# Kernel tuning notes

Measured on AMD Instinct MI355X. Metric: run time of the kernel, lower is better.

Reference implementation:

```python
import jax, jax.numpy as jnp
import numpy as np

D_MODEL = 1024
N_HEADS = 16
D_HEAD = D_MODEL // N_HEADS
D_FF = 4096
B, T = 2, 2048


def setup_inputs() -> dict:
    key = jax.random.key(0)
    ks = jax.random.split(key, 7)
    s = lambda fan_in: 1.0 / np.sqrt(fan_in)
    return {
        "x": jax.random.normal(ks[0], (B, T, D_MODEL), dtype=jnp.float32),
        "ln1_g": jnp.ones((D_MODEL,), jnp.float32),
        "ln1_b": jnp.zeros((D_MODEL,), jnp.float32),
        "w_qkv": jax.random.normal(ks[1], (D_MODEL, 3 * D_MODEL), jnp.float32) * s(D_MODEL),
        "w_proj": jax.random.normal(ks[2], (D_MODEL, D_MODEL), jnp.float32) * s(D_MODEL),
        "ln2_g": jnp.ones((D_MODEL,), jnp.float32),
        "ln2_b": jnp.zeros((D_MODEL,), jnp.float32),
        "w_fc1": jax.random.normal(ks[3], (D_MODEL, D_FF), jnp.float32) * s(D_MODEL),
        "w_fc2": jax.random.normal(ks[4], (D_FF, D_MODEL), jnp.float32) * s(D_FF),
    }


def _layernorm(x, g, b, eps=1e-5):
    mu = jnp.mean(x, axis=-1, keepdims=True)
    var = jnp.var(x, axis=-1, keepdims=True)
    return (x - mu) * jax.lax.rsqrt(var + eps) * g + b


def _attn(x, w_qkv, w_proj):
    Bx, Tx, d = x.shape
    qkv = x @ w_qkv  # [B,T,3d]
    q, k, v = jnp.split(qkv, 3, axis=-1)
    split = lambda t: t.reshape(Bx, Tx, N_HEADS, D_HEAD).transpose(0, 2, 1, 3)
    q, k, v = split(q), split(k), split(v)
    scores = jnp.einsum("bhqd,bhkd->bhqk", q, k) / np.sqrt(D_HEAD).astype(np.float32)
    mask = jnp.tril(jnp.ones((Tx, Tx), dtype=bool))
    scores = jnp.where(mask, scores, -jnp.inf)
    attn = jax.nn.softmax(scores, axis=-1)
    out = jnp.einsum("bhqk,bhkd->bhqd", attn, v)
    out = out.transpose(0, 2, 1, 3).reshape(Bx, Tx, d)
    return out @ w_proj


def reference(x, ln1_g, ln1_b, w_qkv, w_proj, ln2_g, ln2_b, w_fc1, w_fc2):
    x = x + _attn(_layernorm(x, ln1_g, ln1_b), w_qkv, w_proj)
    h = jax.nn.gelu(_layernorm(x, ln2_g, ln2_b) @ w_fc1, approximate=False)
    return x + h @ w_fc2
```

## Files before the change

### kernel.cpp

```cpp
#include <hip/hip_runtime.h>
#include <math.h>

using short8 = __attribute__((ext_vector_type(8))) short;
using f32x4  = __attribute__((ext_vector_type(4))) float;
typedef unsigned short ushort;

__device__ inline ushort f2bf(float f) {
    union { float f; unsigned int i; } v; v.f = f;
    unsigned int x = v.i;
    return (ushort)((x + 0x7FFFu + ((x >> 16) & 1u)) >> 16);
}
__device__ inline void st_out(float* p, float v) { *p = v; }
__device__ inline void st_out(ushort* p, float v) { *p = f2bf(v); }

__device__ inline void gl_lds16(const ushort* g, ushort* l) {
    __builtin_amdgcn_global_load_lds((const __attribute__((address_space(1))) unsigned int*)g,
                                     (__attribute__((address_space(3))) unsigned int*)l, 16, 0, 0);
}
#define MFMA __builtin_amdgcn_mfma_f32_16x16x32_bf16

__global__ __launch_bounds__(256) void ln_kernel(const float* __restrict__ x,
                                                 const float* __restrict__ g,
                                                 const float* __restrict__ b,
                                                 ushort* __restrict__ y) {
    int row = blockIdx.x;
    const float* xr = x + (size_t)row * 1024;
    int t = threadIdx.x;
    float v[4];
    float s = 0.f, s2 = 0.f;
#pragma unroll
    for (int i = 0; i < 4; i++) {
        v[i] = xr[t + i * 256];
        s += v[i]; s2 += v[i] * v[i];
    }
#pragma unroll
    for (int off = 1; off < 64; off <<= 1) {
        s += __shfl_xor(s, off); s2 += __shfl_xor(s2, off);
    }
    __shared__ float ps[8];
    int w = t >> 6;
    if ((t & 63) == 0) { ps[w] = s; ps[4 + w] = s2; }
    __syncthreads();
    s  = ps[0] + ps[1] + ps[2] + ps[3];
    s2 = ps[4] + ps[5] + ps[6] + ps[7];
    float mu   = s * (1.0f / 1024.0f);
    float var  = s2 * (1.0f / 1024.0f) - mu * mu;
    float rinv = rsqrtf(var + 1e-5f);
    ushort* yr = y + (size_t)row * 1024;
#pragma unroll
    for (int i = 0; i < 4; i++) {
        int c = t + i * 256;
        yr[c] = f2bf((v[i] - mu) * rinv * g[c] + b[c]);
    }
}

__global__ __launch_bounds__(256) void wt_kernel(const float* __restrict__ s,
                                                 ushort* __restrict__ d, int K, int N) {
    __shared__ float tile[32][33];
    int n0 = blockIdx.x * 32, k0 = blockIdx.y * 32;
    int tx = threadIdx.x & 31, ty = threadIdx.x >> 5;
#pragma unroll
    for (int i = 0; i < 4; i++)
        tile[ty + i * 8][tx] = s[(size_t)(k0 + ty + i * 8) * N + n0 + tx];
    __syncthreads();
#pragma unroll
    for (int i = 0; i < 4; i++)
        d[(size_t)(n0 + ty + i * 8) * K + k0 + tx] = f2bf(tile[tx][ty + i * 8]);
}

template <int EPI, typename CT>
__global__ __launch_bounds__(256) void gemm_kernel(const ushort* __restrict__ A,
                                                   const ushort* __restrict__ Bt,
                                                   CT* __restrict__ C,
                                                   const float* __restrict__ R,
                                                   ushort* __restrict__ VT,
                                                   int M, int N, int K) {
    __shared__ alignas(16) ushort As[128 * 32];
    __shared__ alignas(16) ushort Bs[128 * 32];
    int t = threadIdx.x, lane = t & 63, w = t >> 6;
    int bm = blockIdx.y * 128, bn = blockIdx.x * 128;
    int wm = (w >> 1) * 64, wn = (w & 1) * 64;
    f32x4 acc[4][4] = {};
    int srow = lane >> 2;
    int schunk = (lane & 3) ^ ((lane >> 3) & 3);
    int rs = lane & 15, qd = lane >> 4;

    for (int k0 = 0; k0 < K; k0 += 32) {
        __syncthreads();
#pragma unroll
        for (int i = 0; i < 2; i++) {
            int idx = w * 2 + i;
            gl_lds16(A  + (size_t)(bm + idx * 16 + srow) * K + k0 + schunk * 8, &As[idx * 512]);
            gl_lds16(Bt + (size_t)(bn + idx * 16 + srow) * K + k0 + schunk * 8, &Bs[idx * 512]);
        }
        __syncthreads();
        short8 af[4], bf[4];
#pragma unroll
        for (int i = 0; i < 4; i++) {
            int ml = wm + i * 16 + rs;
            af[i] = *(const short8*)&As[ml * 32 + ((qd ^ ((ml >> 1) & 3)) * 8)];
            int nl = wn + i * 16 + rs;
            bf[i] = *(const short8*)&Bs[nl * 32 + ((qd ^ ((nl >> 1) & 3)) * 8)];
        }
#pragma unroll
        for (int mi = 0; mi < 4; mi++)
#pragma unroll
            for (int ni = 0; ni < 4; ni++)
                acc[mi][ni] = MFMA(af[mi], bf[ni], acc[mi][ni], 0, 0, 0);
    }
#pragma unroll
    for (int mi = 0; mi < 4; mi++)
#pragma unroll
        for (int ni = 0; ni < 4; ni++) {
            int row = bm + wm + mi * 16 + qd * 4;
            int col = bn + wn + ni * 16 + rs;
            if (EPI == 3) {
                if (col < 2048) {
#pragma unroll
                    for (int r = 0; r < 4; r++)
                        ((ushort*)C)[(size_t)(row + r) * 2048 + col] = f2bf(acc[mi][ni][r]);
                } else {
                    int rel = col - 2048, hh = rel >> 6, dd = rel & 63;
                    ushort tmp[4];
#pragma unroll
                    for (int r = 0; r < 4; r++) tmp[r] = f2bf(acc[mi][ni][r]);
                    size_t base = ((size_t)((row >> 11) * 16 + hh) * 64 + dd) * 2048 + (row & 2047);
                    *(uint2*)&VT[base] = *(uint2*)tmp;
                }
            } else {
#pragma unroll
                for (int r = 0; r < 4; r++) {
                    float v = acc[mi][ni][r];
                    size_t idx = (size_t)(row + r) * N + col;
                    if (EPI == 1) v += R[idx];
                    if (EPI == 2) v = 0.5f * v * (1.0f + erff(v * 0.70710678118f));
                    st_out(&C[idx], v);
                }
            }
        }
}

template <int EPI, typename CT>
__global__ __launch_bounds__(256) void gemm_n64_kernel(const ushort* __restrict__ A,
                                                       const ushort* __restrict__ Bt,
                                                       CT* __restrict__ C,
                                                       const float* __restrict__ R,
                                                       int M, int N, int K, int Kh) {
    __shared__ alignas(16) ushort As[128 * 64];
    __shared__ alignas(16) ushort Bs[64 * 64];
    int t = threadIdx.x, lane = t & 63, w = t >> 6;
    int bm = blockIdx.x * 128, bn = blockIdx.y * 64;
    int kbeg = blockIdx.z * Kh;
    int wm = (w >> 1) * 64, wn = (w & 1) * 32;
    f32x4 acc[4][2] = {};
    int srow = lane >> 3;
    int schunk = (lane & 7) ^ (lane >> 3);
    int rs = lane & 15, qd = lane >> 4;

    for (int k0 = kbeg; k0 < kbeg + Kh; k0 += 64) {
        __syncthreads();
#pragma unroll
        for (int i = 0; i < 4; i++) {
            int rr = w * 32 + i * 8;
            gl_lds16(A + (size_t)(bm + rr + srow) * K + k0 + schunk * 8, &As[rr * 64]);
        }
#pragma unroll
        for (int i = 0; i < 2; i++) {
            int rr = w * 16 + i * 8;
            gl_lds16(Bt + (size_t)(bn + rr + srow) * K + k0 + schunk * 8, &Bs[rr * 64]);
        }
        __syncthreads();
#pragma unroll
        for (int half = 0; half < 2; half++) {
            int cq = qd + half * 4;
            short8 af[4], bfr[2];
#pragma unroll
            for (int i = 0; i < 4; i++) {
                int ml = wm + i * 16 + rs;
                af[i] = *(const short8*)&As[ml * 64 + ((cq ^ (ml & 7)) * 8)];
            }
#pragma unroll
            for (int j = 0; j < 2; j++) {
                int nl = wn + j * 16 + rs;
                bfr[j] = *(const short8*)&Bs[nl * 64 + ((cq ^ (nl & 7)) * 8)];
            }
#pragma unroll
            for (int mi = 0; mi < 4; mi++)
#pragma unroll
                for (int ni = 0; ni < 2; ni++)
                    acc[mi][ni] = MFMA(af[mi], bfr[ni], acc[mi][ni], 0, 0, 0);
        }
    }
#pragma unroll
    for (int mi = 0; mi < 4; mi++)
#pragma unroll
        for (int ni = 0; ni < 2; ni++) {
            int row = bm + wm + mi * 16 + qd * 4;
            int col = bn + wn + ni * 16 + rs;
#pragma unroll
            for (int r = 0; r < 4; r++) {
                float v = acc[mi][ni][r];
                size_t idx = (size_t)(row + r) * N + col;
                if (EPI == 4) {
                    atomicAdd((float*)&C[idx], v);
                } else {
                    if (EPI == 1) v += R[idx];
                    st_out(&C[idx], v);
                }
            }
        }
}

__global__ __launch_bounds__(256) void attn_kernel(const ushort* __restrict__ qk,
                                                   const ushort* __restrict__ vT,
                                                   ushort* __restrict__ outp) {
    __shared__ alignas(16) ushort Ks[128 * 64];
    __shared__ alignas(16) ushort VTs[64 * 128];
    __shared__ alignas(16) ushort Ps[4 * 16 * 136];
    int t = threadIdx.x, lane = t & 63, w = t >> 6;
    int q0 = (int)(gridDim.x - 1 - blockIdx.x) * 64;
    int bh = blockIdx.y, bb = bh >> 4, h = bh & 15;
    const ushort* qkb = qk + (size_t)bb * 2048 * 2048;
    const ushort* qptr = qkb + h * 64;
    const ushort* kptr = qkb + 1024 + h * 64;
    const ushort* vtb  = vT + (size_t)bh * 64 * 2048;
    int rs = lane & 15, qd = lane >> 4;
    int qrow = q0 + w * 16 + rs;
    short8 aq0 = *(const short8*)(qptr + (size_t)qrow * 2048 + qd * 8);
    short8 aq1 = *(const short8*)(qptr + (size_t)qrow * 2048 + 32 + qd * 8);
    f32x4 o_acc[4] = {};
    float l_part[4] = {0.f, 0.f, 0.f, 0.f};
    int myq = q0 + w * 16 + qd * 4;
    int nk = (q0 + 63) / 128 + 1;
    int krl = lane >> 3, kch = lane & 7;
    int vrl = lane >> 4, vch = lane & 15;

    for (int kt = 0; kt < nk; kt++) {
        int k0 = kt * 128;
        __syncthreads();
#pragma unroll
        for (int i = 0; i < 4; i++) {
            int kk = w * 32 + i * 8 + krl;
            gl_lds16(kptr + (size_t)(k0 + kk) * 2048 + ((kch ^ (kk & 7)) * 8), &Ks[(w * 32 + i * 8) * 64]);
            int dd = w * 16 + i * 4 + vrl;
            gl_lds16(vtb + (size_t)dd * 2048 + k0 + ((vch ^ (dd & 15)) * 8), &VTs[(w * 16 + i * 4) * 128]);
        }
        __syncthreads();
        f32x4 s[8];
#pragma unroll
        for (int c = 0; c < 8; c++) {
            int kk = c * 16 + rs;
            short8 kf0 = *(const short8*)&Ks[kk * 64 + ((qd ^ (kk & 7)) * 8)];
            short8 kf1 = *(const short8*)&Ks[kk * 64 + (((qd + 4) ^ (kk & 7)) * 8)];
            f32x4 z = {};
            z = MFMA(aq0, kf0, z, 0, 0, 0);
            z = MFMA(aq1, kf1, z, 0, 0, 0);
            s[c] = z;
        }
        bool lastt = (kt == nk - 1);
#pragma unroll
        for (int c = 0; c < 8; c++) {
            int kk = k0 + c * 16 + rs;
#pragma unroll
            for (int r = 0; r < 4; r++) {
                float p = __expf(s[c][r] * 0.125f);
                if (lastt && (kk > myq + r)) p = 0.f;
                s[c][r] = p;
                l_part[r] += p;
            }
        }
#pragma unroll
        for (int r = 0; r < 4; r++)
#pragma unroll
            for (int c = 0; c < 8; c++)
                Ps[(w * 16 + qd * 4 + r) * 136 + c * 16 + rs] = f2bf(s[c][r]);
        short8 ap[4];
#pragma unroll
        for (int kc = 0; kc < 4; kc++)
            ap[kc] = *(const short8*)&Ps[(w * 16 + rs) * 136 + kc * 32 + qd * 8];
#pragma unroll
        for (int dt = 0; dt < 4; dt++) {
            int dd = dt * 16 + rs;
#pragma unroll
            for (int kc = 0; kc < 4; kc++) {
                int g = kc * 4 + qd;
                short8 bv = *(const short8*)&VTs[dd * 128 + ((g ^ (dd & 15)) * 8)];
                o_acc[dt] = MFMA(ap[kc], bv, o_acc[dt], 0, 0, 0);
            }
        }
    }
#pragma unroll
    for (int r = 0; r < 4; r++)
#pragma unroll
        for (int off = 1; off < 16; off <<= 1)
            l_part[r] += __shfl_xor(l_part[r], off);
#pragma unroll
    for (int dt = 0; dt < 4; dt++)
#pragma unroll
        for (int r = 0; r < 4; r++)
            outp[(size_t)(bb * 2048 + myq + r) * 1024 + h * 64 + dt * 16 + rs] = f2bf(o_acc[dt][r] / l_part[r]);
}

extern "C" void kernel_launch(void* const* d_in, const int* in_sizes, int n_in,
                              void* d_out, int out_size, void* d_ws, size_t ws_size,
                              hipStream_t stream) {
    const float* x     = (const float*)d_in[0];
    const float* ln1g  = (const float*)d_in[1];
    const float* ln1b  = (const float*)d_in[2];
    const float* wqkv  = (const float*)d_in[3];
    const float* wproj = (const float*)d_in[4];
    const float* ln2g  = (const float*)d_in[5];
    const float* ln2b  = (const float*)d_in[6];
    const float* wfc1  = (const float*)d_in[7];
    const float* wfc2  = (const float*)d_in[8];
    float* out = (float*)d_out;
    char* ws = (char*)d_ws;
    const size_t MB = 1024 * 1024;

    ushort* wbufA = (ushort*)(ws);
    ushort* lnbuf = (ushort*)(ws + 8 * MB);
    ushort* qk    = (ushort*)(ws + 16 * MB);
    ushort* vT    = (ushort*)(ws + 32 * MB);
    const int Rr = 4096;

    ln_kernel<<<Rr, 256, 0, stream>>>(x, ln1g, ln1b, lnbuf);
    wt_kernel<<<dim3(3072 / 32, 1024 / 32), 256, 0, stream>>>(wqkv, wbufA, 1024, 3072);
    gemm_kernel<3, ushort><<<dim3(3072 / 128, Rr / 128), 256, 0, stream>>>(lnbuf, wbufA, qk, nullptr, vT, Rr, 3072, 1024);
    attn_kernel<<<dim3(2048 / 64, 32), 256, 0, stream>>>(qk, vT, lnbuf);
    wt_kernel<<<dim3(1024 / 32, 1024 / 32), 256, 0, stream>>>(wproj, wbufA, 1024, 1024);
    gemm_n64_kernel<1, float><<<dim3(Rr / 128, 1024 / 64, 1), 256, 0, stream>>>(lnbuf, wbufA, out, x, Rr, 1024, 1024, 1024);
    ln_kernel<<<Rr, 256, 0, stream>>>(out, ln2g, ln2b, lnbuf);
    wt_kernel<<<dim3(4096 / 32, 1024 / 32), 256, 0, stream>>>(wfc1, wbufA, 1024, 4096);

    if (ws_size >= 56 * MB) {
        ushort* hmid  = qk;
        ushort* wbufB = (ushort*)(ws + 48 * MB);
        wt_kernel<<<dim3(1024 / 32, 4096 / 32), 256, 0, stream>>>(wfc2, wbufB, 4096, 1024);
        gemm_kernel<2, ushort><<<dim3(4096 / 128, Rr / 128), 256, 0, stream>>>(lnbuf, wbufA, hmid, nullptr, nullptr, Rr, 4096, 1024);
        gemm_n64_kernel<4, float><<<dim3(Rr / 128, 1024 / 64, 2), 256, 0, stream>>>(hmid, wbufB, out, nullptr, Rr, 1024, 4096, 2048);
    } else {
        ushort* hmid  = qk;
        ushort* wbufB = (ushort*)(ws + 32 * MB);
        wt_kernel<<<dim3(1024 / 32, 4096 / 32), 256, 0, stream>>>(wfc2, wbufB, 4096, 1024);
        for (int hf = 0; hf < 2; hf++) {
            const ushort* lnh = lnbuf + (size_t)hf * 2048 * 1024;
            float* outh = out + (size_t)hf * 2048 * 1024;
            gemm_kernel<2, ushort><<<dim3(4096 / 128, 2048 / 128), 256, 0, stream>>>(lnh, wbufA, hmid, nullptr, nullptr, 2048, 4096, 1024);
            gemm_n64_kernel<4, float><<<dim3(2048 / 128, 1024 / 64, 2), 256, 0, stream>>>(hmid, wbufB, outh, nullptr, 2048, 1024, 4096, 2048);
        }
    }
}
```

Before: 397.3 us.

## Split attention over key blocks with atomic accumulation; widen GEMM K tile to 64

The attention kernel now splits each query tile's key range into chunks of up to four key blocks along a third grid dimension. Partial unnormalized outputs and row sums are accumulated with float atomics into zeroed buffers, and a separate finalize kernel normalizes them and converts to bf16. This is meant to fix load imbalance from causal masking and add parallelism, at the cost of memsets, atomic traffic and an extra pass. Separately, the main GEMM loads a K tile of 64 per iteration with a new 8-way swizzle, which halves the number of barrier pairs.

```diff
diff --git a/kernel.cpp b/kernel.cpp
--- a/kernel.cpp
+++ b/kernel.cpp
@@ -75,38 +75,42 @@
                                                    const float* __restrict__ R,
                                                    ushort* __restrict__ VT,
                                                    int M, int N, int K) {
-    __shared__ alignas(16) ushort As[128 * 32];
-    __shared__ alignas(16) ushort Bs[128 * 32];
+    __shared__ alignas(16) ushort As[128 * 64];
+    __shared__ alignas(16) ushort Bs[128 * 64];
     int t = threadIdx.x, lane = t & 63, w = t >> 6;
     int bm = blockIdx.y * 128, bn = blockIdx.x * 128;
     int wm = (w >> 1) * 64, wn = (w & 1) * 64;
     f32x4 acc[4][4] = {};
-    int srow = lane >> 2;
-    int schunk = (lane & 3) ^ ((lane >> 3) & 3);
+    int srow = lane >> 3;
+    int schunk = (lane & 7) ^ (lane >> 3);
     int rs = lane & 15, qd = lane >> 4;
 
-    for (int k0 = 0; k0 < K; k0 += 32) {
-        __syncthreads();
-#pragma unroll
-        for (int i = 0; i < 2; i++) {
-            int idx = w * 2 + i;
-            gl_lds16(A  + (size_t)(bm + idx * 16 + srow) * K + k0 + schunk * 8, &As[idx * 512]);
-            gl_lds16(Bt + (size_t)(bn + idx * 16 + srow) * K + k0 + schunk * 8, &Bs[idx * 512]);
-        }
-        __syncthreads();
-        short8 af[4], bf[4];
+    for (int k0 = 0; k0 < K; k0 += 64) {
+        __syncthreads();
 #pragma unroll
         for (int i = 0; i < 4; i++) {
-            int ml = wm + i * 16 + rs;
-            af[i] = *(const short8*)&As[ml * 32 + ((qd ^ ((ml >> 1) & 3)) * 8)];
-            int nl = wn + i * 16 + rs;
-            bf[i] = *(const short8*)&Bs[nl * 32 + ((qd ^ ((nl >> 1) & 3)) * 8)];
-        }
-#pragma unroll
-        for (int mi = 0; mi < 4; mi++)
-#pragma unroll
-            for (int ni = 0; ni < 4; ni++)
-                acc[mi][ni] = MFMA(af[mi], bf[ni], acc[mi][ni], 0, 0, 0);
+            int rr = w * 32 + i * 8;
+            gl_lds16(A  + (size_t)(bm + rr + srow) * K + k0 + schunk * 8, &As[rr * 64]);
+            gl_lds16(Bt + (size_t)(bn + rr + srow) * K + k0 + schunk * 8, &Bs[rr * 64]);
+        }
+        __syncthreads();
+#pragma unroll
+        for (int half = 0; half < 2; half++) {
+            int cq = qd + half * 4;
+            short8 af[4], bf[4];
+#pragma unroll
+            for (int i = 0; i < 4; i++) {
+                int ml = wm + i * 16 + rs;
+                af[i] = *(const short8*)&As[ml * 64 + ((cq ^ (ml & 7)) * 8)];
+                int nl = wn + i * 16 + rs;
+                bf[i] = *(const short8*)&Bs[nl * 64 + ((cq ^ (nl & 7)) * 8)];
+            }
+#pragma unroll
+            for (int mi = 0; mi < 4; mi++)
+#pragma unroll
+                for (int ni = 0; ni < 4; ni++)
+                    acc[mi][ni] = MFMA(af[mi], bf[ni], acc[mi][ni], 0, 0, 0);
+        }
     }
 #pragma unroll
     for (int mi = 0; mi < 4; mi++)
@@ -213,12 +217,18 @@
 
 __global__ __launch_bounds__(256) void attn_kernel(const ushort* __restrict__ qk,
                                                    const ushort* __restrict__ vT,
-                                                   ushort* __restrict__ outp) {
+                                                   float* __restrict__ accO,
+                                                   float* __restrict__ accL) {
+    int qi = blockIdx.x;
+    int nk = qi / 2 + 1;
+    int t0 = blockIdx.z * 4;
+    if (t0 >= nk) return;
+    int t1 = min(t0 + 4, nk);
     __shared__ alignas(16) ushort Ks[128 * 64];
     __shared__ alignas(16) ushort VTs[64 * 128];
     __shared__ alignas(16) ushort Ps[4 * 16 * 136];
     int t = threadIdx.x, lane = t & 63, w = t >> 6;
-    int q0 = (int)(gridDim.x - 1 - blockIdx.x) * 64;
+    int q0 = qi * 64;
     int bh = blockIdx.y, bb = bh >> 4, h = bh & 15;
     const ushort* qkb = qk + (size_t)bb * 2048 * 2048;
     const ushort* qptr = qkb + h * 64;
@@ -231,11 +241,10 @@
     f32x4 o_acc[4] = {};
     float l_part[4] = {0.f, 0.f, 0.f, 0.f};
     int myq = q0 + w * 16 + qd * 4;
-    int nk = (q0 + 63) / 128 + 1;
     int krl = lane >> 3, kch = lane & 7;
     int vrl = lane >> 4, vch = lane & 15;
 
-    for (int kt = 0; kt < nk; kt++) {
+    for (int kt = t0; kt < t1; kt++) {
         int k0 = kt * 128;
         __syncthreads();
 #pragma unroll
@@ -298,7 +307,22 @@
     for (int dt = 0; dt < 4; dt++)
 #pragma unroll
         for (int r = 0; r < 4; r++)
-            outp[(size_t)(bb * 2048 + myq + r) * 1024 + h * 64 + dt * 16 + rs] = f2bf(o_acc[dt][r] / l_part[r]);
+            atomicAdd(&accO[(size_t)(bb * 2048 + myq + r) * 1024 + h * 64 + dt * 16 + rs], o_acc[dt][r]);
+    if (rs == 0)
+#pragma unroll
+        for (int r = 0; r < 4; r++)
+            atomicAdd(&accL[(size_t)(bb * 2048 + myq + r) * 16 + h], l_part[r]);
+}
+
+__global__ __launch_bounds__(256) void attn_fin_kernel(const float* __restrict__ accO,
+                                                       const float* __restrict__ accL,
+                                                       ushort* __restrict__ outp) {
+    int row = blockIdx.x;
+    int c0 = threadIdx.x * 4;
+    float inv = 1.0f / accL[row * 16 + (c0 >> 6)];
+    float4 o = *(const float4*)(accO + (size_t)row * 1024 + c0);
+    ushort r4[4] = { f2bf(o.x * inv), f2bf(o.y * inv), f2bf(o.z * inv), f2bf(o.w * inv) };
+    *(uint2*)(outp + (size_t)row * 1024 + c0) = *(uint2*)r4;
 }
 
 extern "C" void kernel_launch(void* const* d_in, const int* in_sizes, int n_in,
@@ -321,12 +345,17 @@
     ushort* lnbuf = (ushort*)(ws + 8 * MB);
     ushort* qk    = (ushort*)(ws + 16 * MB);
     ushort* vT    = (ushort*)(ws + 32 * MB);
+    float*  accL  = (float*)(ws + 40 * MB);
+    float*  accO  = out;
     const int Rr = 4096;
 
     ln_kernel<<<Rr, 256, 0, stream>>>(x, ln1g, ln1b, lnbuf);
     wt_kernel<<<dim3(3072 / 32, 1024 / 32), 256, 0, stream>>>(wqkv, wbufA, 1024, 3072);
     gemm_kernel<3, ushort><<<dim3(3072 / 128, Rr / 128), 256, 0, stream>>>(lnbuf, wbufA, qk, nullptr, vT, Rr, 3072, 1024);
-    attn_kernel<<<dim3(2048 / 64, 32), 256, 0, stream>>>(qk, vT, lnbuf);
+    hipMemsetAsync(accO, 0, (size_t)Rr * 1024 * 4, stream);
+    hipMemsetAsync(accL, 0, (size_t)Rr * 16 * 4, stream);
+    attn_kernel<<<dim3(32, 32, 4), 256, 0, stream>>>(qk, vT, accO, accL);
+    attn_fin_kernel<<<Rr, 256, 0, stream>>>(accO, accL, lnbuf);
     wt_kernel<<<dim3(1024 / 32, 1024 / 32), 256, 0, stream>>>(wproj, wbufA, 1024, 1024);
     gemm_n64_kernel<1, float><<<dim3(Rr / 128, 1024 / 64, 1), 256, 0, stream>>>(lnbuf, wbufA, out, x, Rr, 1024, 1024, 1024);
     ln_kernel<<<Rr, 256, 0, stream>>>(out, ln2g, ln2b, lnbuf);
```

Result: no change. 404.8 us (+1.9%).
